# Performance work log

Measured on AMD Instinct MI355X. Metric: run time of the kernel, lower is better.

The kernel has to match this reference:

```python
import jax, jax.numpy as jnp
import numpy as np

B, S, D, G, N_ORIG = 4, 4096, 512, 64, 4096
EPS_NORM = 1e-12   # F.normalize eps
EPS_MERGE = 1e-8   # merge-weight eps


def setup_inputs() -> dict:
    key = jax.random.key(0)
    k1, k2, k3 = jax.random.split(key, 3)
    x = jax.random.normal(k1, (B, S, D), dtype=jnp.float32)
    source = jax.random.uniform(k2, (B, S, N_ORIG), dtype=jnp.float32)
    position_ids = jnp.arange(B * S, dtype=jnp.int64).reshape(B, S)
    W = jax.random.normal(k3, (D, G), dtype=jnp.float32) * 0.05  # group_proj weight (no bias)
    return {"x": x, "source": source, "position_ids": position_ids,
            "r": 1024, "window_size": 16, "W": W}


def _token_merge(x, source, position_ids, r, window_size, W):
    Bb, Ss, Dd = x.shape
    r = min(r, Ss // 2)
    idx = jnp.arange(Ss, dtype=jnp.int32)
    # local candidate pairs: |i-j| = d for d in 1..window_size-1
    pi = jnp.concatenate([idx[:Ss - d] for d in range(1, min(window_size, Ss))])
    pj = jnp.concatenate([idx[d:] for d in range(1, min(window_size, Ss))])

    g = x @ W                                   # (B,S,G)
    norms = jnp.linalg.norm(g, axis=-1)         # (B,S)
    gn = g / jnp.maximum(norms, EPS_NORM)[..., None]
    sim = jnp.einsum('bpg,bpg->bp', gn[:, pi], gn[:, pj])  # (B,P)

    def greedy(sim_b):
        # deterministic order: score DESC, i ASC, j ASC
        order = jnp.lexsort((pj, pi, -sim_b))
        oi, oj = pi[order], pj[order]

        def step(carry, ij):
            used, partner, cnt = carry
            i, j = ij
            take = (cnt < r) & (~used[i]) & (~used[j])
            used = used.at[i].set(used[i] | take).at[j].set(used[j] | take)
            partner = partner.at[i].set(jnp.where(take, j, partner[i]))
            cnt = cnt + take.astype(jnp.int32)
            return (used, partner, cnt), None

        init = (jnp.zeros(Ss, bool), jnp.full(Ss, -1, jnp.int32), jnp.int32(0))
        (used, partner, cnt), _ = jax.lax.scan(step, init, (oi, oj))
        return partner  # partner[i] = j if pair (i,j) selected, else -1

    partner = jax.vmap(greedy)(sim)  # (B,S)

    def merge(xb, sb, pb, partner_b, norms_b):
        sel = partner_b >= 0
        pj_safe = jnp.where(sel, partner_b, idx)
        wi = norms_b
        wj = jnp.where(sel, norms_b[pj_safe], 0.0)
        merged = (wi[:, None] * xb + wj[:, None] * xb[pj_safe]) / (wi + wj + EPS_MERGE)[:, None]
        x_m = jnp.where(sel[:, None], merged, xb)
        s_m = sb + jnp.where(sel, 1.0, 0.0)[:, None] * sb[pj_safe]
        # drop the second token of each merged pair, preserving order
        skip_idx = jnp.where(sel, partner_b, Ss)
        skip = jnp.zeros(Ss, bool).at[skip_idx].set(True, mode='drop')
        keep = jnp.argsort(skip.astype(jnp.int8), stable=True)[: Ss - r]
        return x_m[keep], s_m[keep], pb[keep]

    return jax.vmap(merge)(x, source, position_ids, partner, norms)


def reference(x, source, position_ids, r, window_size, W):
    return _token_merge(x, source, position_ids, r, window_size, W)
```

## Files before the change

### kernel.cpp

```cpp
#include <hip/hip_runtime.h>

#define BATCH 4
#define SLEN 4096
#define DDIM 512
#define GDIM 64
#define NORIG 4096
#define WMAX 15
#define RSEL 1024
#define KEEP (SLEN - RSEL)
#define NTOK (BATCH * SLEN)
#define PEEL_ROUNDS 256
#define LDSL 8

#define OFF_LISTS ((size_t)0)
#define OFF_GN    ((size_t)0)
#define OFF_SIMST ((size_t)8388608)
#define OFF_NORMS ((size_t)10485760)
#define OFF_KT    ((size_t)10584064)
#define OFF_PJR   ((size_t)10633216)
#define OFF_WIR   ((size_t)10682368)
#define OFF_WJR   ((size_t)10731520)
#define WS_NEEDED ((size_t)10780672)

#define OUTX_OFF 0
#define OUTS_OFF 6291456
#define OUTP_OFF 56623104

__global__ __launch_bounds__(256) void k_proj(const float* __restrict__ x,
                                              const float* __restrict__ Wm,
                                              double* __restrict__ gn,
                                              float* __restrict__ norms) {
  __shared__ float xs[16 * DDIM];
  int base = blockIdx.x * 16;
  const float4* src = (const float4*)(x + (size_t)base * DDIM);
  float4* dstv = (float4*)xs;
  for (int idx = threadIdx.x; idx < 16 * DDIM / 4; idx += 256) dstv[idx] = src[idx];
  __syncthreads();
  int lane = threadIdx.x & 63;
  int wv = threadIdx.x >> 6;
  double acc0 = 0, acc1 = 0, acc2 = 0, acc3 = 0;
  const float* xw = xs + wv * 4 * DDIM;
  for (int d = 0; d < DDIM; ++d) {
    double wval = (double)Wm[d * GDIM + lane];
    acc0 += (double)xw[d] * wval;
    acc1 += (double)xw[DDIM + d] * wval;
    acc2 += (double)xw[2 * DDIM + d] * wval;
    acc3 += (double)xw[3 * DDIM + d] * wval;
  }
  double accs[4] = {acc0, acc1, acc2, acc3};
  for (int k = 0; k < 4; ++k) {
    double a = accs[k];
    double ss = a * a;
    for (int o = 32; o >= 1; o >>= 1) ss += __shfl_xor(ss, o, 64);
    double nrm = sqrt(ss);
    int tok = base + wv * 4 + k;
    if (lane == 0) norms[tok] = (float)nrm;
    double denom = nrm > 1e-12 ? nrm : 1e-12;
    gn[(size_t)tok * GDIM + lane] = a / denom;
  }
}

__global__ __launch_bounds__(256) void k_sims(const double* __restrict__ gn,
                                              double* __restrict__ simsT) {
  int blk = blockIdx.x;
  int b = blk >> 6;
  int t0 = (blk & 63) * 64;
  int nrows = min(64 + WMAX, SLEN - t0);
  __shared__ double gs[(64 + WMAX) * GDIM];
  const double* src = gn + ((size_t)b * SLEN + t0) * GDIM;
  for (int idx = threadIdx.x; idx < nrows * GDIM; idx += 256) gs[idx] = src[idx];
  __syncthreads();
  int lane = threadIdx.x & 63, wv = threadIdx.x >> 6;
  for (int s = wv; s < 64 * WMAX; s += 4) {
    int il = s & 63, d = (s >> 6) + 1;
    int i = t0 + il;
    if (i + d < SLEN) {
      double p = gs[il * GDIM + lane] * gs[(il + d) * GDIM + lane];
      for (int o = 32; o >= 1; o >>= 1) p += __shfl_xor(p, o, 64);
      if (lane == 0) simsT[((size_t)(b * SLEN + i)) * 16 + d] = p;
    }
  }
}

__global__ __launch_bounds__(256) void k_lists(const double* __restrict__ simsT,
                                               signed char* __restrict__ lists8) {
  __shared__ signed char stage[4][32];
  int wave = threadIdx.x >> 6, lane = threadIdx.x & 63;
  int t = blockIdx.x * 4 + wave;
  int b = t >> 12, tt = t & (SLEN - 1);
  const double* sb = simsT + (size_t)b * SLEN * 16;
  int d = (lane >> 1) + 1;
  int side = lane & 1;
  bool valid = (lane < 30) && (side == 0 ? (tt + d < SLEN) : (tt - d >= 0));
  unsigned long long key = 0ULL;
  unsigned int code = 0xFFFFu;
  signed char delta = 0;
  if (valid) {
    int i = (side == 0) ? tt : (tt - d);
    double s = sb[(size_t)i * 16 + d];
    unsigned long long bits = (unsigned long long)__double_as_longlong(s);
    key = (bits & 0x8000000000000000ULL) ? ~bits : (bits | 0x8000000000000000ULL);
    code = (unsigned int)((i << 4) | d);
    delta = (side == 0) ? (signed char)d : (signed char)(-d);
  }
  int rank = 0;
#pragma clang loop unroll(disable)
  for (int q = 0; q < 30; ++q) {
    unsigned long long kq = __shfl(key, q, 64);
    unsigned int cq = __shfl(code, q, 64);
    if (kq != 0ULL && (kq > key || (kq == key && cq < code))) rank++;
  }
  if (lane < 32) stage[wave][lane] = 0;
  if (valid) stage[wave][rank] = delta;
  if (lane < 32) lists8[(size_t)t * 32 + lane] = stage[wave][lane];
}

__global__ __launch_bounds__(1024) void k_match(const signed char* __restrict__ lists8,
                                                const double* __restrict__ simsT_all,
                                                const float* __restrict__ norms,
                                                int* __restrict__ kt, int* __restrict__ pjr,
                                                float* __restrict__ wir, float* __restrict__ wjr,
                                                float* __restrict__ out_pos) {
  int b = blockIdx.x;
  const signed char* lb = lists8 + (size_t)b * SLEN * 32;
  const double* simsT = simsT_all + (size_t)b * SLEN * 16;
  __shared__ __align__(16) unsigned char big[32768];
  __shared__ signed char bp[SLEN];
  __shared__ unsigned char used[SLEN];
  __shared__ unsigned char cur[SLEN];
  __shared__ unsigned short takenCode[2048];
  __shared__ unsigned char meta[SLEN];
  __shared__ int takenCnt, baseCnt;
  __shared__ int sharedB, sharedNeed, sdone, allAccept;
  __shared__ int memberCnt;
  __shared__ int wTot[16], wOff[16];
  signed char* l8 = (signed char*)big;
  int tid = threadIdx.x;

#pragma clang loop unroll(disable)
  for (int t = tid; t < SLEN; t += 1024) {
    unsigned long long v = *(const unsigned long long*)(lb + (size_t)t * 32);
    *(unsigned long long*)(l8 + t * LDSL) = v;
    bp[t] = (signed char)(v & 0xFF);
    used[t] = 0; cur[t] = 0; meta[t] = 0;
  }
  if (tid == 0) takenCnt = 0;
  __syncthreads();

#pragma clang loop unroll(disable)
  for (int round = 0; round < PEEL_ROUNDS; ++round) {
    if (tid == 0) baseCnt = takenCnt;
    __syncthreads();
#pragma clang loop unroll(disable)
    for (int t = tid; t < SLEN; t += 1024) {
      int dlt = bp[t];
      if (dlt > 0 && !used[t]) {
        int j = t + dlt;
        if (!used[j] && bp[j] == (signed char)(-dlt)) {
          int idx = atomicAdd(&takenCnt, 1);
          if (idx < 2048) takenCode[idx] = (unsigned short)((t << 4) | dlt);
          used[t] = 1; used[j] = 1;
        }
      }
    }
    __syncthreads();
    int newCnt = takenCnt;
    if (newCnt == baseCnt) break;
#pragma clang loop unroll(disable)
    for (int t = tid; t < SLEN; t += 1024) {
      if (used[t]) { bp[t] = 0; continue; }
      int dlt = bp[t];
      if (dlt == 0) continue;
      int p = t + dlt;
      int cc = cur[t];
#pragma clang loop unroll(disable)
      while (dlt != 0 && used[p]) {
        ++cc;
        dlt = (cc < LDSL) ? l8[t * LDSL + cc]
            : ((cc < 32) ? lb[(size_t)t * 32 + cc] : (signed char)0);
        p = t + dlt;
      }
      cur[t] = (unsigned char)cc;
      bp[t] = (signed char)dlt;
    }
    __syncthreads();
  }

  unsigned long long* key = (unsigned long long*)big;
  unsigned short* codeA = (unsigned short*)(big + 16384);
  unsigned char* state = (unsigned char*)(big + 20480);
  unsigned int* hist = (unsigned int*)(big + 22528);
  unsigned int* bcum = (unsigned int*)(big + 23552);
  unsigned int* wsum = (unsigned int*)(big + 24576);
  unsigned short* memberIdx = (unsigned short*)(big + 24704);
  int m = min(takenCnt, 2048);
  __syncthreads();
#pragma clang loop unroll(disable)
  for (int k = tid; k < m; k += 1024) {
    unsigned short c = takenCode[k];
    codeA[k] = c;
    state[k] = 0;
    double s = simsT[(size_t)(c >> 4) * 16 + (c & 15)];
    unsigned long long bits = (unsigned long long)__double_as_longlong(s);
    key[k] = (bits & 0x8000000000000000ULL) ? ~bits : (bits | 0x8000000000000000ULL);
  }
  if (tid == 0) { sharedNeed = RSEL; sdone = 0; allAccept = (m <= RSEL); memberCnt = 0; }
  __syncthreads();

  if (!allAccept) {
#pragma clang loop unroll(disable)
    for (int pass = 0; pass < 8; ++pass) {
      if (tid < 256) hist[tid] = 0;
      __syncthreads();
      int sh = 56 - 8 * pass;
#pragma clang loop unroll(disable)
      for (int k = tid; k < m; k += 1024)
        if (!state[k]) atomicAdd(&hist[(unsigned int)(key[k] >> sh) & 0xFFu], 1u);
      __syncthreads();
      unsigned int v = 0, inc = 0;
      int lane = tid & 63, w = tid >> 6;
      if (tid < 256) {
        v = hist[255 - tid];
        inc = v;
        for (int o = 1; o < 64; o <<= 1) { unsigned int n = __shfl_up(inc, o, 64); if (lane >= o) inc += n; }
        if (lane == 63) wsum[w] = inc;
      }
      __syncthreads();
      if (tid < 256) {
        unsigned int off = 0;
        for (int ww = 0; ww < w; ++ww) off += wsum[ww];
        unsigned int incl = inc + off;
        bcum[255 - tid] = incl - v;
      }
      __syncthreads();
      if (tid < 256) {
        int bkt = 255 - tid;
        unsigned int ag = bcum[bkt];
        unsigned int need = (unsigned int)sharedNeed;
        if (ag < need && ag + hist[bkt] >= need) sharedB = bkt;
      }
      __syncthreads();
      int B = sharedB;
      unsigned int needInB = (unsigned int)sharedNeed - bcum[B];
#pragma clang loop unroll(disable)
      for (int k = tid; k < m; k += 1024) {
        if (!state[k]) {
          unsigned int bv = (unsigned int)(key[k] >> sh) & 0xFFu;
          if ((int)bv > B) state[k] = 1;
          else if ((int)bv < B) state[k] = 2;
        }
      }
      __syncthreads();
      if (tid == 0) {
        sharedNeed = (int)needInB;
        if (hist[B] == needInB) sdone = 1;
      }
      __syncthreads();
      if (sdone) break;
    }
  }
  __syncthreads();

  if (allAccept || sdone) {
#pragma clang loop unroll(disable)
    for (int k = tid; k < m; k += 1024) if (!state[k]) state[k] = 1;
  } else {
#pragma clang loop unroll(disable)
    for (int k = tid; k < m; k += 1024)
      if (!state[k]) { int idx = atomicAdd(&memberCnt, 1); memberIdx[idx] = (unsigned short)k; }
    __syncthreads();
    int mc = memberCnt;
    unsigned int need = (unsigned int)sharedNeed;
#pragma clang loop unroll(disable)
    for (int z = tid; z < mc; z += 1024) {
      int k = memberIdx[z];
      unsigned short ck = codeA[k];
      unsigned int wr = 0;
#pragma clang loop unroll(disable)
      for (int q2 = 0; q2 < mc; ++q2) if (codeA[memberIdx[q2]] < ck) wr++;
      if (wr < need) state[k] = 1;
    }
  }
  __syncthreads();
#pragma clang loop unroll(disable)
  for (int k = tid; k < m; k += 1024) {
    if (state[k] == 1) {
      unsigned short ck = codeA[k];
      int i = ck >> 4, d = ck & 15;
      meta[i] = (unsigned char)d;
      meta[i + d] = 0x80;
    }
  }
  __syncthreads();
  int cnt = 0; unsigned char kf[4];
  int tbase = tid * 4;
  for (int u = 0; u < 4; ++u) { kf[u] = (meta[tbase + u] & 0x80) ? 0 : 1; cnt += kf[u]; }
  int lane = tid & 63, wv = tid >> 6;
  int incl = cnt;
  for (int o = 1; o < 64; o <<= 1) { int n = __shfl_up(incl, o, 64); if (lane >= o) incl += n; }
  if (lane == 63) wTot[wv] = incl;
  __syncthreads();
  if (tid < 16) {
    int v2 = wTot[tid];
    for (int o = 1; o < 16; o <<= 1) { int n = __shfl_up(v2, o, 64); if (lane >= o) v2 += n; }
    wOff[tid] = v2 - wTot[tid];
  }
  __syncthreads();
  int pos = wOff[wv] + (incl - cnt);
  for (int u = 0; u < 4; ++u) {
    int t = tbase + u;
    if (kf[u]) {
      if (pos < KEEP) {
        int orow = b * KEEP + pos;
        kt[orow] = t;
        int d = meta[t] & 15;
        pjr[orow] = d ? (t + d) : -1;
        wir[orow] = norms[b * SLEN + t];
        wjr[orow] = d ? norms[b * SLEN + t + d] : 0.0f;
        out_pos[orow] = (float)(b * SLEN + t);
      }
      pos++;
    }
  }
}

__global__ __launch_bounds__(256) void k_gather(const float* __restrict__ x,
                                                const float* __restrict__ src,
                                                const int* __restrict__ kt, const int* __restrict__ pjr,
                                                const float* __restrict__ wir, const float* __restrict__ wjr,
                                                float* __restrict__ outx, float* __restrict__ outs) {
  int orow = blockIdx.x;
  int b = orow / KEEP;
  int t = kt[orow], pj = pjr[orow];
  int gi = min(max(b * SLEN + t, 0), NTOK - 1);
  int gj = min(b * SLEN + min(max(pj, 0), SLEN - 1), NTOK - 1);
  int c = threadIdx.x;
  if (c < 128) {
    const float4* xi = (const float4*)(x + (size_t)gi * DDIM);
    float4 v = xi[c];
    if (pj >= 0) {
      const float4* xj = (const float4*)(x + (size_t)gj * DDIM);
      float4 u = xj[c];
      float wi = wir[orow], wj = wjr[orow];
      float inv = 1.0f / (wi + wj + 1e-8f);
      v.x = (wi * v.x + wj * u.x) * inv;
      v.y = (wi * v.y + wj * u.y) * inv;
      v.z = (wi * v.z + wj * u.z) * inv;
      v.w = (wi * v.w + wj * u.w) * inv;
    }
    ((float4*)(outx + (size_t)orow * DDIM))[c] = v;
  }
  const float4* si = (const float4*)(src + (size_t)gi * NORIG);
  float4* o = (float4*)(outs + (size_t)orow * NORIG);
  if (pj >= 0) {
    const float4* sj = (const float4*)(src + (size_t)gj * NORIG);
    for (int u = 0; u < 4; ++u) {
      int c2 = c + u * 256;
      float4 a = si[c2], bb = sj[c2];
      a.x += bb.x; a.y += bb.y; a.z += bb.z; a.w += bb.w;
      o[c2] = a;
    }
  } else {
    for (int u = 0; u < 4; ++u) { int c2 = c + u * 256; o[c2] = si[c2]; }
  }
}

extern "C" void kernel_launch(void* const* d_in, const int* in_sizes, int n_in,
                              void* d_out, int out_size, void* d_ws, size_t ws_size,
                              hipStream_t stream) {
  if (ws_size < WS_NEEDED) return;

  const float* x = (const float*)d_in[0];
  const float* source = (const float*)d_in[1];
  const float* Wm = (const float*)d_in[5];

  char* ws = (char*)d_ws;
  double* gn = (double*)(ws + OFF_GN);
  double* simsT = (double*)(ws + OFF_SIMST);
  float* norms = (float*)(ws + OFF_NORMS);
  signed char* lists8 = (signed char*)(ws + OFF_LISTS);
  int* kt = (int*)(ws + OFF_KT);
  int* pjr = (int*)(ws + OFF_PJR);
  float* wir = (float*)(ws + OFF_WIR);
  float* wjr = (float*)(ws + OFF_WJR);

  float* out = (float*)d_out;
  float* outx = out + OUTX_OFF;
  float* outs = out + OUTS_OFF;
  float* outp = out + OUTP_OFF;

  k_proj<<<(BATCH * SLEN) / 16, 256, 0, stream>>>(x, Wm, gn, norms);
  k_sims<<<BATCH * (SLEN / 64), 256, 0, stream>>>(gn, simsT);
  k_lists<<<NTOK / 4, 256, 0, stream>>>(simsT, lists8);
  k_match<<<BATCH, 1024, 0, stream>>>(lists8, simsT, norms, kt, pjr, wir, wjr, outp);
  k_gather<<<BATCH * KEEP, 256, 0, stream>>>(x, source, kt, pjr, wir, wjr, outx, outs);
}
```

Measured before the change: 354.9 us.

## Use nontemporal gather I/O, widen LDS candidate lists, early-exit radix select

The gather kernel now uses nontemporal vector loads and stores for the x and source rows, aiming to avoid cache pollution on the large streaming copy that dominates traffic. The match kernel copies 16 bytes of each candidate list into LDS instead of 8, doubling the shared buffer to 64 KB. The radix-select loop also exits early once the straddling bucket holds 128 or fewer entries, and resolves that bucket with a quadratic rank over score and code. These changes raise LDS use per block and change the select tie-break logic, which could affect correctness if the rank comparison is wrong.

```diff
diff --git a/kernel.cpp b/kernel.cpp
--- a/kernel.cpp
+++ b/kernel.cpp
@@ -10,7 +10,9 @@
 #define KEEP (SLEN - RSEL)
 #define NTOK (BATCH * SLEN)
 #define PEEL_ROUNDS 256
-#define LDSL 8
+#define LDSL 16
+
+typedef float __attribute__((ext_vector_type(4))) f32x4;
 
 #define OFF_LISTS ((size_t)0)
 #define OFF_GN    ((size_t)0)
@@ -124,14 +126,14 @@
   int b = blockIdx.x;
   const signed char* lb = lists8 + (size_t)b * SLEN * 32;
   const double* simsT = simsT_all + (size_t)b * SLEN * 16;
-  __shared__ __align__(16) unsigned char big[32768];
+  __shared__ __align__(16) unsigned char big[65536];
   __shared__ signed char bp[SLEN];
   __shared__ unsigned char used[SLEN];
   __shared__ unsigned char cur[SLEN];
   __shared__ unsigned short takenCode[2048];
   __shared__ unsigned char meta[SLEN];
   __shared__ int takenCnt, baseCnt;
-  __shared__ int sharedB, sharedNeed, sdone, allAccept;
+  __shared__ int sharedB, sharedNeed, sdone, allAccept, smallStraddle;
   __shared__ int memberCnt;
   __shared__ int wTot[16], wOff[16];
   signed char* l8 = (signed char*)big;
@@ -139,9 +141,11 @@
 
 #pragma clang loop unroll(disable)
   for (int t = tid; t < SLEN; t += 1024) {
-    unsigned long long v = *(const unsigned long long*)(lb + (size_t)t * 32);
-    *(unsigned long long*)(l8 + t * LDSL) = v;
-    bp[t] = (signed char)(v & 0xFF);
+    const unsigned long long* lp = (const unsigned long long*)(lb + (size_t)t * 32);
+    unsigned long long v0 = lp[0], v1 = lp[1];
+    unsigned long long* dp = (unsigned long long*)(l8 + t * LDSL);
+    dp[0] = v0; dp[1] = v1;
+    bp[t] = (signed char)(v0 & 0xFF);
     used[t] = 0; cur[t] = 0; meta[t] = 0;
   }
   if (tid == 0) takenCnt = 0;
@@ -204,7 +208,7 @@
     unsigned long long bits = (unsigned long long)__double_as_longlong(s);
     key[k] = (bits & 0x8000000000000000ULL) ? ~bits : (bits | 0x8000000000000000ULL);
   }
-  if (tid == 0) { sharedNeed = RSEL; sdone = 0; allAccept = (m <= RSEL); memberCnt = 0; }
+  if (tid == 0) { sharedNeed = RSEL; sdone = 0; allAccept = (m <= RSEL); smallStraddle = 0; memberCnt = 0; }
   __syncthreads();
 
   if (!allAccept) {
@@ -254,9 +258,10 @@
       if (tid == 0) {
         sharedNeed = (int)needInB;
         if (hist[B] == needInB) sdone = 1;
-      }
-      __syncthreads();
-      if (sdone) break;
+        else if (hist[B] <= 128) smallStraddle = 1;
+      }
+      __syncthreads();
+      if (sdone || smallStraddle) break;
     }
   }
   __syncthreads();
@@ -274,10 +279,15 @@
 #pragma clang loop unroll(disable)
     for (int z = tid; z < mc; z += 1024) {
       int k = memberIdx[z];
+      unsigned long long kk = key[k];
       unsigned short ck = codeA[k];
       unsigned int wr = 0;
 #pragma clang loop unroll(disable)
-      for (int q2 = 0; q2 < mc; ++q2) if (codeA[memberIdx[q2]] < ck) wr++;
+      for (int q2 = 0; q2 < mc; ++q2) {
+        int q = memberIdx[q2];
+        unsigned long long kq = key[q];
+        if (kq > kk || (kq == kk && codeA[q] < ck)) wr++;
+      }
       if (wr < need) state[k] = 1;
     }
   }
@@ -336,32 +346,33 @@
   int gj = min(b * SLEN + min(max(pj, 0), SLEN - 1), NTOK - 1);
   int c = threadIdx.x;
   if (c < 128) {
-    const float4* xi = (const float4*)(x + (size_t)gi * DDIM);
-    float4 v = xi[c];
+    const f32x4* xi = (const f32x4*)(x + (size_t)gi * DDIM);
+    f32x4 v = __builtin_nontemporal_load(&xi[c]);
     if (pj >= 0) {
-      const float4* xj = (const float4*)(x + (size_t)gj * DDIM);
-      float4 u = xj[c];
+      const f32x4* xj = (const f32x4*)(x + (size_t)gj * DDIM);
+      f32x4 u = __builtin_nontemporal_load(&xj[c]);
       float wi = wir[orow], wj = wjr[orow];
       float inv = 1.0f / (wi + wj + 1e-8f);
-      v.x = (wi * v.x + wj * u.x) * inv;
-      v.y = (wi * v.y + wj * u.y) * inv;
-      v.z = (wi * v.z + wj * u.z) * inv;
-      v.w = (wi * v.w + wj * u.w) * inv;
-    }
-    ((float4*)(outx + (size_t)orow * DDIM))[c] = v;
-  }
-  const float4* si = (const float4*)(src + (size_t)gi * NORIG);
-  float4* o = (float4*)(outs + (size_t)orow * NORIG);
+      v = (v * wi + u * wj) * inv;
+    }
+    __builtin_nontemporal_store(v, (f32x4*)(outx + (size_t)orow * DDIM) + c);
+  }
+  const f32x4* si = (const f32x4*)(src + (size_t)gi * NORIG);
+  f32x4* o = (f32x4*)(outs + (size_t)orow * NORIG);
   if (pj >= 0) {
-    const float4* sj = (const float4*)(src + (size_t)gj * NORIG);
+    const f32x4* sj = (const f32x4*)(src + (size_t)gj * NORIG);
     for (int u = 0; u < 4; ++u) {
       int c2 = c + u * 256;
-      float4 a = si[c2], bb = sj[c2];
-      a.x += bb.x; a.y += bb.y; a.z += bb.z; a.w += bb.w;
-      o[c2] = a;
+      f32x4 a = __builtin_nontemporal_load(&si[c2]);
+      f32x4 bb = __builtin_nontemporal_load(&sj[c2]);
+      __builtin_nontemporal_store(a + bb, &o[c2]);
     }
   } else {
-    for (int u = 0; u < 4; ++u) { int c2 = c + u * 256; o[c2] = si[c2]; }
+    for (int u = 0; u < 4; ++u) {
+      int c2 = c + u * 256;
+      f32x4 a = __builtin_nontemporal_load(&si[c2]);
+      __builtin_nontemporal_store(a, &o[c2]);
+    }
   }
 }
 
```

New measurement: 346.9 us. 2.2% less time.
